# Optimization experiments

Measured on AMD Instinct MI355X. Metric: run time of the kernel, lower is better.

## Reference

```python
import jax, jax.numpy as jnp
import numpy as np

RHO = 1000.0  # seawater density used to convert wind stress to acceleration


def setup_inputs() -> dict:
    key = jax.random.key(0)
    k1, k2 = jax.random.split(key)
    Nforcing = 1440  # 60 days of hourly forcing
    TAx = (0.05 * jax.random.normal(k1, (Nforcing,), dtype=jnp.float32) + 0.08)
    TAy = 0.05 * jax.random.normal(k2, (Nforcing,), dtype=jnp.float32)
    pk = jnp.array([-3.9, -11.5], dtype=jnp.float32)  # K0 ~ 1/50m, K1 ~ 1e-5 s^-1
    fc = jnp.float32(1e-4)  # Coriolis frequency
    return {"pk": pk, "TAx": TAx, "TAy": TAy, "fc": fc,
            "t0": 0, "t1": 5184000, "dt": 60, "dt_forcing": 3600}


def _forward(pk, TAx, TAy, fc, t0, t1, dt, dt_forcing):
    nsub = dt_forcing // dt            # substeps per forcing step (static python int)
    Nf = (t1 - t0) // dt_forcing       # number of forcing steps
    n = TAx.shape[0]
    K = jnp.exp(pk)
    # Ekman (equilibrium) component, complex current Ce = K0*T / (K1 + i*fc)
    T = (TAx + 1j * TAy) / RHO
    Ce = K[0] * T / (K[1] + 1j * fc)
    Ue, Ve = jnp.real(Ce), jnp.imag(Ce)
    # NOTE: original uses self.dt (model dt, not dt_forcing) as gradient spacing
    dCedt = jnp.gradient(Ce, dt)
    dUedt, dVedt = jnp.real(dCedt), jnp.imag(dCedt)
    dtf = jnp.float32(dt)
    K1 = K[1]
    # interpolation weights aa = (it mod nsub)/nsub = iin/nsub, same for every outer step
    aas = jnp.arange(nsub, dtype=jnp.float32) / nsub

    def outer(carry, iout):
        # original: itsup = -1 if iout+1 >= len(TAx), which wraps to last element
        itsup = jnp.where(iout + 1 >= n, n - 1, iout + 1)
        dUe0, dUe1 = dUedt[iout], dUedt[itsup]
        dVe0, dVe1 = dVedt[iout], dVedt[itsup]

        def inner(c, aa):
            u, v = c
            dUe = (1.0 - aa) * dUe0 + aa * dUe1
            dVe = (1.0 - aa) * dVe0 + aa * dVe1
            du = -K1 * u + fc * v - dUe
            dv = -K1 * v - fc * u - dVe
            return (u + dtf * du, v + dtf * dv), None

        c, _ = jax.lax.scan(inner, carry, aas)
        return c, c

    init = (jnp.float32(0.0), jnp.float32(0.0))
    _, (us, vs) = jax.lax.scan(outer, init, jnp.arange(Nf))
    # original writes U[iout+1]: index Nf is out-of-bounds and dropped by .at[].set,
    # so the saved trajectory is the state shifted by one step with the last write dropped
    Unio = jnp.concatenate([jnp.zeros((1,), us.dtype), us[:-1]])
    Vnio = jnp.concatenate([jnp.zeros((1,), vs.dtype), vs[:-1]])
    return Ue + Unio, Ve + Vnio


def reference(pk, TAx, TAy, fc, t0, t1, dt, dt_forcing):
    return _forward(pk, TAx, TAy, fc, t0, t1, dt, dt_forcing)
```

## Files before the change

### kernel.cpp

```cpp
#include <hip/hip_runtime.h>
#include <hip/hip_bf16.h>


#define LSEG 24

__global__ void jslab_kernel(const float* __restrict__ pk,
                             const float* __restrict__ TAx,
                             const float* __restrict__ TAy,
                             const float* __restrict__ fc_p,
                             const int* __restrict__ dt_p,
                             const int* __restrict__ dtf_p,
                             float* __restrict__ out,
                             int n, int Nf) {
    extern __shared__ double sm[];
    double* CeR = sm;
    double* CeI = sm + n;
    double* FR  = sm + 2 * n;
    double* FI  = sm + 2 * n + Nf;

    const int tid = threadIdx.x;
    const int nt  = blockDim.x;

    const double K0  = exp((double)pk[0]);
    const double K1  = exp((double)pk[1]);
    const double fc  = (double)fc_p[0];
    const int    dt  = dt_p[0];
    const int    dtF = dtf_p[0];
    const int    nsub = dtF / dt;
    const double dtf = (double)dt;

    const double den  = K1 * K1 + fc * fc;
    const double invR =  K1 / den;
    const double invI = -fc / den;
    const double RHO = 1000.0;

    for (int i = tid; i < n; i += nt) {
        double tr = (double)TAx[i] / RHO;
        double ti = (double)TAy[i] / RHO;
        CeR[i] = K0 * (tr * invR - ti * invI);
        CeI[i] = K0 * (tr * invI + ti * invR);
    }

    const double Ar = 1.0 - dtf * K1;
    const double Ai = -dtf * fc;
    double Br = 1.0, Bi = 0.0;
    double s0r = 0.0, s0i = 0.0, s1r = 0.0, s1i = 0.0;
    for (int j = 0; j < nsub; ++j) {
        double aa = (double)((float)j / (float)nsub);
        double n0r = Ar * s0r - Ai * s0i + (1.0 - aa);
        double n0i = Ar * s0i + Ai * s0r;
        s0r = n0r; s0i = n0i;
        double n1r = Ar * s1r - Ai * s1i + aa;
        double n1i = Ar * s1i + Ai * s1r;
        s1r = n1r; s1i = n1i;
        double nbr = Br * Ar - Bi * Ai;
        double nbi = Br * Ai + Bi * Ar;
        Br = nbr; Bi = nbi;
    }
    const double P0r = -dtf * s0r, P0i = -dtf * s0i;
    const double P1r = -dtf * s1r, P1i = -dtf * s1i;

    __syncthreads();

    for (int i = tid; i < Nf; i += nt) {
        int i0 = i     < n ? i     : n - 1;
        int i1 = i + 1 < n ? i + 1 : n - 1;
        double d0r, d0i, d1r, d1i;
        {
            int k = i0;
            if (k == 0)          { d0r = (CeR[1] - CeR[0]) / dtf;           d0i = (CeI[1] - CeI[0]) / dtf; }
            else if (k == n - 1) { d0r = (CeR[n-1] - CeR[n-2]) / dtf;       d0i = (CeI[n-1] - CeI[n-2]) / dtf; }
            else                 { d0r = (CeR[k+1] - CeR[k-1]) / (2.0*dtf); d0i = (CeI[k+1] - CeI[k-1]) / (2.0*dtf); }
        }
        {
            int k = i1;
            if (k == 0)          { d1r = (CeR[1] - CeR[0]) / dtf;           d1i = (CeI[1] - CeI[0]) / dtf; }
            else if (k == n - 1) { d1r = (CeR[n-1] - CeR[n-2]) / dtf;       d1i = (CeI[n-1] - CeI[n-2]) / dtf; }
            else                 { d1r = (CeR[k+1] - CeR[k-1]) / (2.0*dtf); d1i = (CeI[k+1] - CeI[k-1]) / (2.0*dtf); }
        }
        FR[i] = P0r * d0r - P0i * d0i + P1r * d1r - P1i * d1i;
        FI[i] = P0r * d0i + P0i * d0r + P1r * d1i + P1i * d1r;
    }
    __syncthreads();

    if (tid < 64) {
        const int lane = tid;
        const int base = lane * LSEG;

        double pr = 0.0, pi = 0.0;
        #pragma unroll
        for (int j = 0; j < LSEG; ++j) {
            int i = base + j;
            double fr = (i < Nf) ? FR[i] : 0.0;
            double fi = (i < Nf) ? FI[i] : 0.0;
            double nr = Br * pr - Bi * pi + fr;
            double ni = Br * pi + Bi * pr + fi;
            pr = nr; pi = ni;
        }

        double wr = 1.0, wi = 0.0;
        #pragma unroll
        for (int k = 0; k < LSEG; ++k) {
            double nr = wr * Br - wi * Bi;
            double ni = wr * Bi + wi * Br;
            wr = nr; wi = ni;
        }

        double xr = pr, xi = pi;
        double cwr = wr, cwi = wi;
        #pragma unroll
        for (int d = 1; d < 64; d <<= 1) {
            double yr = __shfl_up(xr, d, 64);
            double yi = __shfl_up(xi, d, 64);
            if (lane >= d) {
                xr += cwr * yr - cwi * yi;
                xi += cwr * yi + cwi * yr;
            }
            double nr = cwr * cwr - cwi * cwi;
            double ni = 2.0 * cwr * cwi;
            cwr = nr; cwi = ni;
        }

        double cr = __shfl_up(xr, 1, 64);
        double ci = __shfl_up(xi, 1, 64);
        if (lane == 0) { cr = 0.0; ci = 0.0; }

        #pragma unroll
        for (int j = 0; j < LSEG; ++j) {
            int i = base + j;
            if (i < Nf) {
                out[i]      = (float)(CeR[i] + cr);
                out[Nf + i] = (float)(CeI[i] + ci);
                double nr = Br * cr - Bi * ci + FR[i];
                double ni = Br * ci + Bi * cr + FI[i];
                cr = nr; ci = ni;
            }
        }
    }
}

extern "C" void kernel_launch(void* const* d_in, const int* in_sizes, int n_in,
                              void* d_out, int out_size, void* d_ws, size_t ws_size,
                              hipStream_t stream) {
    const float* pk   = (const float*)d_in[0];
    const float* TAx  = (const float*)d_in[1];
    const float* TAy  = (const float*)d_in[2];
    const float* fc   = (const float*)d_in[3];
    const int*   dt   = (const int*)d_in[6];
    const int*   dtF  = (const int*)d_in[7];
    float* out = (float*)d_out;

    const int n  = in_sizes[1];
    const int Nf = out_size / 2;

    size_t shmem = (size_t)(2 * n + 2 * Nf) * sizeof(double);
    jslab_kernel<<<dim3(1), dim3(256), shmem, stream>>>(
        pk, TAx, TAy, fc, dt, dtF, out, n, Nf);
}
```

Baseline: 79.19 us.

## Fuse forcing computation into single-wave scan and keep forcing in registers

```diff
diff --git a/kernel.cpp b/kernel.cpp
--- a/kernel.cpp
+++ b/kernel.cpp
@@ -4,29 +4,26 @@
 
 #define LSEG 24
 
-__global__ void jslab_kernel(const float* __restrict__ pk,
-                             const float* __restrict__ TAx,
-                             const float* __restrict__ TAy,
-                             const float* __restrict__ fc_p,
-                             const int* __restrict__ dt_p,
-                             const int* __restrict__ dtf_p,
-                             float* __restrict__ out,
-                             int n, int Nf) {
+__global__ __launch_bounds__(64)
+void jslab_kernel(const float* __restrict__ pk,
+                  const float* __restrict__ TAx,
+                  const float* __restrict__ TAy,
+                  const float* __restrict__ fc_p,
+                  const int* __restrict__ dt_p,
+                  const int* __restrict__ dtf_p,
+                  float* __restrict__ out,
+                  int n, int Nf) {
     extern __shared__ double sm[];
     double* CeR = sm;
     double* CeI = sm + n;
-    double* FR  = sm + 2 * n;
-    double* FI  = sm + 2 * n + Nf;
 
-    const int tid = threadIdx.x;
-    const int nt  = blockDim.x;
+    const int lane = threadIdx.x;
 
     const double K0  = exp((double)pk[0]);
     const double K1  = exp((double)pk[1]);
     const double fc  = (double)fc_p[0];
     const int    dt  = dt_p[0];
-    const int    dtF = dtf_p[0];
-    const int    nsub = dtF / dt;
+    const int    nsub = dtf_p[0] / dt;
     const double dtf = (double)dt;
 
     const double den  = K1 * K1 + fc * fc;
@@ -34,7 +31,7 @@
     const double invI = -fc / den;
     const double RHO = 1000.0;
 
-    for (int i = tid; i < n; i += nt) {
+    for (int i = lane; i < n; i += 64) {
         double tr = (double)TAx[i] / RHO;
         double ti = (double)TAy[i] / RHO;
         CeR[i] = K0 * (tr * invR - ti * invI);
@@ -62,79 +59,72 @@
 
     __syncthreads();
 
-    for (int i = tid; i < Nf; i += nt) {
-        int i0 = i     < n ? i     : n - 1;
-        int i1 = i + 1 < n ? i + 1 : n - 1;
-        double d0r, d0i, d1r, d1i;
-        {
-            int k = i0;
-            if (k == 0)          { d0r = (CeR[1] - CeR[0]) / dtf;           d0i = (CeI[1] - CeI[0]) / dtf; }
-            else if (k == n - 1) { d0r = (CeR[n-1] - CeR[n-2]) / dtf;       d0i = (CeI[n-1] - CeI[n-2]) / dtf; }
-            else                 { d0r = (CeR[k+1] - CeR[k-1]) / (2.0*dtf); d0i = (CeI[k+1] - CeI[k-1]) / (2.0*dtf); }
+    const int base = lane * LSEG;
+
+    auto dCe = [&](int k, double& dr, double& di) {
+        if (k == 0)          { dr = (CeR[1] - CeR[0]) / dtf;           di = (CeI[1] - CeI[0]) / dtf; }
+        else if (k == n - 1) { dr = (CeR[n-1] - CeR[n-2]) / dtf;       di = (CeI[n-1] - CeI[n-2]) / dtf; }
+        else                 { dr = (CeR[k+1] - CeR[k-1]) / (2.0*dtf); di = (CeI[k+1] - CeI[k-1]) / (2.0*dtf); }
+    };
+
+    double fRr[LSEG], fIr[LSEG];
+    double pr = 0.0, pi = 0.0;
+    double d0r = 0.0, d0i = 0.0;
+    if (base < Nf) dCe(base, d0r, d0i);
+    #pragma unroll
+    for (int j = 0; j < LSEG; ++j) {
+        int i = base + j;
+        double fr = 0.0, fi = 0.0;
+        if (i < Nf) {
+            int i1 = (i + 1 < n) ? i + 1 : n - 1;
+            double d1r, d1i;
+            dCe(i1, d1r, d1i);
+            fr = P0r * d0r - P0i * d0i + P1r * d1r - P1i * d1i;
+            fi = P0r * d0i + P0i * d0r + P1r * d1i + P1i * d1r;
+            d0r = d1r; d0i = d1i;
         }
-        {
-            int k = i1;
-            if (k == 0)          { d1r = (CeR[1] - CeR[0]) / dtf;           d1i = (CeI[1] - CeI[0]) / dtf; }
-            else if (k == n - 1) { d1r = (CeR[n-1] - CeR[n-2]) / dtf;       d1i = (CeI[n-1] - CeI[n-2]) / dtf; }
-            else                 { d1r = (CeR[k+1] - CeR[k-1]) / (2.0*dtf); d1i = (CeI[k+1] - CeI[k-1]) / (2.0*dtf); }
+        fRr[j] = fr; fIr[j] = fi;
+        double nr = Br * pr - Bi * pi + fr;
+        double ni = Br * pi + Bi * pr + fi;
+        pr = nr; pi = ni;
+    }
+
+    double wr = 1.0, wi = 0.0;
+    #pragma unroll
+    for (int k = 0; k < LSEG; ++k) {
+        double nr = wr * Br - wi * Bi;
+        double ni = wr * Bi + wi * Br;
+        wr = nr; wi = ni;
+    }
+
+    double xr = pr, xi = pi;
+    double cwr = wr, cwi = wi;
+    #pragma unroll
+    for (int d = 1; d < 64; d <<= 1) {
+        double yr = __shfl_up(xr, d, 64);
+        double yi = __shfl_up(xi, d, 64);
+        if (lane >= d) {
+            xr += cwr * yr - cwi * yi;
+            xi += cwr * yi + cwi * yr;
         }
-        FR[i] = P0r * d0r - P0i * d0i + P1r * d1r - P1i * d1i;
-        FI[i] = P0r * d0i + P0i * d0r + P1r * d1i + P1i * d1r;
+        double nr = cwr * cwr - cwi * cwi;
+        double ni = 2.0 * cwr * cwi;
+        cwr = nr; cwi = ni;
     }
-    __syncthreads();
 
-    if (tid < 64) {
-        const int lane = tid;
-        const int base = lane * LSEG;
+    double cr = __shfl_up(xr, 1, 64);
+    double ci = __shfl_up(xi, 1, 64);
+    if (lane == 0) { cr = 0.0; ci = 0.0; }
 
-        double pr = 0.0, pi = 0.0;
-        #pragma unroll
-        for (int j = 0; j < LSEG; ++j) {
-            int i = base + j;
-            double fr = (i < Nf) ? FR[i] : 0.0;
-            double fi = (i < Nf) ? FI[i] : 0.0;
-            double nr = Br * pr - Bi * pi + fr;
-            double ni = Br * pi + Bi * pr + fi;
-            pr = nr; pi = ni;
-        }
-
-        double wr = 1.0, wi = 0.0;
-        #pragma unroll
-        for (int k = 0; k < LSEG; ++k) {
-            double nr = wr * Br - wi * Bi;
-            double ni = wr * Bi + wi * Br;
-            wr = nr; wi = ni;
-        }
-
-        double xr = pr, xi = pi;
-        double cwr = wr, cwi = wi;
-        #pragma unroll
-        for (int d = 1; d < 64; d <<= 1) {
-            double yr = __shfl_up(xr, d, 64);
-            double yi = __shfl_up(xi, d, 64);
-            if (lane >= d) {
-                xr += cwr * yr - cwi * yi;
-                xi += cwr * yi + cwi * yr;
-            }
-            double nr = cwr * cwr - cwi * cwi;
-            double ni = 2.0 * cwr * cwi;
-            cwr = nr; cwi = ni;
-        }
-
-        double cr = __shfl_up(xr, 1, 64);
-        double ci = __shfl_up(xi, 1, 64);
-        if (lane == 0) { cr = 0.0; ci = 0.0; }
-
-        #pragma unroll
-        for (int j = 0; j < LSEG; ++j) {
-            int i = base + j;
-            if (i < Nf) {
-                out[i]      = (float)(CeR[i] + cr);
-                out[Nf + i] = (float)(CeI[i] + ci);
-                double nr = Br * cr - Bi * ci + FR[i];
-                double ni = Br * ci + Bi * cr + FI[i];
-                cr = nr; ci = ni;
-            }
+    #pragma unroll
+    for (int j = 0; j < LSEG; ++j) {
+        int i = base + j;
+        if (i < Nf) {
+            out[i]      = (float)(CeR[i] + cr);
+            out[Nf + i] = (float)(CeI[i] + ci);
+            double nr = Br * cr - Bi * ci + fRr[j];
+            double ni = Br * ci + Bi * cr + fIr[j];
+            cr = nr; ci = ni;
         }
     }
 }
@@ -153,7 +143,7 @@
     const int n  = in_sizes[1];
     const int Nf = out_size / 2;
 
-    size_t shmem = (size_t)(2 * n + 2 * Nf) * sizeof(double);
-    jslab_kernel<<<dim3(1), dim3(256), shmem, stream>>>(
+    size_t shmem = (size_t)(2 * n) * sizeof(double);
+    jslab_kernel<<<dim3(1), dim3(64), shmem, stream>>>(
         pk, TAx, TAy, fc, dt, dtF, out, n, Nf);
 }
```

Result: slower. 87.05 us (+9.9%).
